# Kernel optimization log

Measured on AMD Instinct MI355X. Metric: run time of the kernel, lower is better.

The kernel has to match this reference:

```python
import jax, jax.numpy as jnp
import numpy as np
import math

B = 2048
INPUT_SIZE = 1024
OUTPUT_SIZE = 512
SPONGE = 1024
ACT = 256
REC = 256
STORE = ACT + REC  # 512
DEPTH = 8
BDEPTH = 10
NEUTRAL_C = 1.0
SQRT2 = math.sqrt(2.0)


def _make_structure():
    # Deterministic stand-in for the module's random.sample-based recall wiring.
    rng = np.random.RandomState(0)
    half = (SPONGE + 1) // 2
    shuffle_perm = np.array([i // 2 + (i % 2) * half for i in range(SPONGE)], dtype=np.int64)
    unused = []
    recall = []
    for i in range(DEPTH):
        unused.extend(range(i * STORE, (i + 1) * STORE))
        sel = rng.choice(len(unused), size=REC, replace=False)
        sel_set = set(sel.tolist())
        recall.append([unused[k] for k in sorted(sel_set)])
        unused = [u for k, u in enumerate(unused) if k not in sel_set]
    out_mem = np.array(sorted(unused), dtype=np.int64)  # 2048 leftover memory columns
    bf_size = len(out_mem) + SPONGE  # 3072
    bf_depth = int(math.ceil(math.log2(bf_size)))  # 12
    bf_half = (bf_size + 1) // 2
    bf_perm = np.array([i // 2 + (i % 2) * bf_half for i in range(bf_size)], dtype=np.int64)
    return shuffle_perm, np.array(recall, dtype=np.int64), out_mem, bf_perm, bf_size, bf_depth


def setup_inputs() -> dict:
    key = jax.random.key(0)
    ks = jax.random.split(key, 6)
    shuffle_perm, recall_idx, out_mem_idx, bf_perm, bf_size, bf_depth = _make_structure()
    return {
        "X": jax.random.normal(ks[0], (B, INPUT_SIZE), jnp.float32),
        "scales": jnp.ones((INPUT_SIZE,), jnp.float32),
        "angles": jax.random.uniform(ks[1], (DEPTH, BDEPTH, SPONGE // 2), jnp.float32) * (2 * math.pi),
        "act_bias": jax.random.normal(ks[2], (DEPTH, ACT), jnp.float32),
        "act_activation": jax.random.normal(ks[3], (DEPTH, ACT), jnp.float32),
        "act_curvature": jax.random.normal(ks[4], (DEPTH, ACT), jnp.float32),
        "bf_angles": jax.random.uniform(ks[5], (bf_depth, bf_size // 2), jnp.float32) * (2 * math.pi),
        "shuffle_perm": jnp.asarray(shuffle_perm),
        "recall_idx": jnp.asarray(recall_idx),
        "output_mem_idx": jnp.asarray(out_mem_idx),
        "bf_perm": jnp.asarray(bf_perm),
    }


def _base_activation(x, c):
    # In the source, `a` is overwritten with torch.tensor(1.0), so a == 1.
    t = (math.pi / 4) / c
    y0 = (1.0 / c) * (1.0 / SQRT2 - math.cos(math.pi / 2))  # = 1/(c*sqrt(2))
    m0 = math.sin(math.pi / 2)  # = 1
    y1 = (1.0 / c) * (1.0 / SQRT2 - 1.0)
    m1 = math.sin(0.0)  # = 0
    mid = (1.0 / c) * (1.0 / SQRT2 - jnp.cos(math.pi / 4 + c * x))
    return jnp.where(x > t, y0 + m0 * (x - t), jnp.where(x < -t, y1 + m1 * (x + t), mid))


def _butterfly(x, angles, perm):
    # angles: [n_layers, exch]; shuffle -> Givens rotation per pair, extra passthrough
    exch = angles.shape[1]
    for j in range(angles.shape[0]):
        s = x[:, perm]
        x1, x2 = s[:, :exch], s[:, exch:2 * exch]
        ca, sa = jnp.cos(angles[j]), jnp.sin(angles[j])
        x = jnp.concatenate([ca * x1 + sa * x2, -sa * x1 + ca * x2, s[:, 2 * exch:]], axis=1)
    return x


def reference(X, scales, angles, act_bias, act_activation, act_curvature, bf_angles,
              shuffle_perm, recall_idx, output_mem_idx, bf_perm):
    Xs = X * scales
    sponge = Xs[:, :SPONGE]  # input_size == sponge_size: no zero pad, memory[0] is empty
    mem = jnp.zeros((Xs.shape[0], DEPTH * STORE), Xs.dtype)
    for i in range(DEPTH):
        sponge = _butterfly(sponge, angles[i], shuffle_perm)
        x1 = sponge[:, STORE:STORE + ACT] + act_bias[i]  # activation_position == store_size
        c = 0.5 * NEUTRAL_C * (act_curvature[i] + jnp.sqrt(act_curvature[i] ** 2 + 1.0))
        ap = _base_activation(x1, c)
        am = _base_activation(-x1, c)
        act_out = jnp.stack([ap, am], axis=2).reshape(ap.shape[0], 2 * ACT)  # interleave +/-
        mem = mem.at[:, i * STORE:(i + 1) * STORE].set(sponge[:, :STORE])
        recall = mem[:, recall_idx[i]]  # indices only address already-filled columns
        # [act_out | sponge[store:act_pos] (empty) | sponge[act_pos+ACT:] | recall]
        sponge = jnp.concatenate([act_out, sponge[:, STORE + ACT:], recall], axis=1)
    pre = jnp.concatenate([mem[:, output_mem_idx], sponge], axis=1)  # [B, 3072]
    out = _butterfly(pre, bf_angles, bf_perm)
    return out[:, :OUTPUT_SIZE]
```

## Files before the change

### kernel.cpp

```cpp
#include <hip/hip_runtime.h>
#include <math.h>

#define NB 2048
#define DEPTH 8

#define FTAB_OFF    0
#define BF01_OFF    81920
#define BFF_OFF     88064
#define ACT4_OFF    98304
#define PHYSA_OFF   106496
#define PHYSR_OFF   110592
#define PHYSO2_OFF  112640

#define MB0 4608
#define MB1 6656

#define SBAR() asm volatile("s_waitcnt lgkmcnt(0)\n\ts_barrier" ::: "memory")

__global__ void setup_kernel(const float* __restrict__ angles,
                             const float* __restrict__ bf_angles,
                             const float* __restrict__ act_bias,
                             const float* __restrict__ act_curv,
                             const int* __restrict__ recall_idx,
                             const int* __restrict__ out_mem_idx,
                             float* __restrict__ ws) {
    __shared__ int physL[4096];
    __shared__ int rcl[2048];
    __shared__ int oml[2048];
    if (blockIdx.x < 200) {
        int id = blockIdx.x * 256 + threadIdx.x;
        if (id < 40960) {
            int w = id & 3, t = (id >> 2) & 255, dg = id >> 10;
            int d = dg / 5, g = dg - 5 * d;
            int a = 2 * (t & 127) + (t >> 7);
            int pair = (w == 0) ? a : (w == 1) ? (a + 256)
                     : (w == 2) ? (2 * a) : (2 * a + 1);
            int st = 2 * g + (w >> 1);
            float ang = angles[(d * 10 + st) * 512 + pair];
            float s, c; __sincosf(ang, &s, &c);
            ws[FTAB_OFF + 2 * id]     = c;
            ws[FTAB_OFF + 2 * id + 1] = s;
        } else if (id < 44032) {
            int e = id - 40960;
            int w = e & 3; int ti = e >> 2;
            int t = ti / 3; int i = ti - 3 * t;
            int a = t + 256 * i;
            int pair = (w == 0) ? a : (w == 1) ? (a + 768)
                     : (w == 2) ? (2 * a) : (2 * a + 1);
            int stage = (w < 2) ? 0 : 1;
            float ang = bf_angles[stage * 1536 + pair];
            float s, c; __sincosf(ang, &s, &c);
            ws[BF01_OFF + 2 * e]     = c;
            ws[BF01_OFF + 2 * e + 1] = s;
        } else if (id < 49152) {
            int e = id - 44032;
            int f = e >> 10; int rem = e & 1023; int t = rem >> 2; int w = rem & 3;
            int P;
            if (f == 0) P = 3 * t;
            else if (f < 4) { int k = 8 - 2 * f;
                              P = ((t >> (2 * f)) * (768 >> k)) + (t & ((256 >> k) - 1)); }
            else P = t;
            int pair = (w == 0) ? P : (w == 1) ? (P + 768)
                     : (w == 2) ? (2 * P) : (2 * P + 1);
            int stage = (w < 2) ? (2 + 2 * f) : (3 + 2 * f);
            float ang = bf_angles[stage * 1536 + pair];
            float s, c; __sincosf(ang, &s, &c);
            ws[BFF_OFF + 2 * e]     = c;
            ws[BFF_OFF + 2 * e + 1] = s;
        } else if (id < 51200) {
            int ida = id - 49152;
            float cu = act_curv[ida];
            float c  = 0.5f * (cu + sqrtf(cu * cu + 1.0f));
            ((float4*)(ws + ACT4_OFF))[ida] =
                make_float4(act_bias[ida], c, 1.0f / c, 0.0f);
        }
    } else {
        int tid = threadIdx.x;
        for (int e = tid; e < 2048; e += 256) rcl[e] = recall_idx[e];
        for (int e = tid; e < 2048; e += 256) oml[e] = out_mem_idx[e];
        for (int e = tid; e < 512; e += 256) physL[e] = e;
        __syncthreads();
        for (int d = 1; d < 8; ++d) {
            for (int j = tid; j < 512; j += 256) {
                int p;
                if (j < 256) p = 256 + d * 256 + j;
                else          p = physL[rcl[(d - 1) * 256 + (j - 256)]];
                physL[512 * d + j] = p;
            }
            __syncthreads();
        }
        int* pa = (int*)(ws + PHYSA_OFF);
        for (int e = tid; e < 2048; e += 256) {
            int d = e >> 8, t = e & 255;
            int a = 2 * (t & 127) + (t >> 7);
            pa[2 * e]     = 2 * physL[d * 512 + 2 * a];
            pa[2 * e + 1] = 2 * physL[d * 512 + 2 * a + 1];
        }
        int* pr = (int*)(ws + PHYSR_OFF);
        for (int e = tid; e < 2048; e += 256)
            pr[e] = 2 * physL[rcl[e]];
        int* po = (int*)(ws + PHYSO2_OFF);
        for (int e = tid; e < 3072; e += 256) {
            int tt = e / 12; int r = e - 12 * tt; int i = r >> 2; int k = r & 3;
            int a = tt + 256 * i;
            int tl2 = a >> 1, th2 = a & 1;
            int pos = tl2 + 1536 * th2 + 384 * k;
            po[e] = (pos < 2048) ? 2 * physL[oml[pos]]
                                 : MB0 + 2 * (pos - 2048);
        }
    }
}

__device__ __forceinline__ float actf(float x, float c, float ic) {
    const float is2 = 0.70710678118654752f;
    float tt = 0.78539816339744831f * ic;
    float y0 = is2 * ic;
    float y1 = (is2 - 1.0f) * ic;
    float mid = ic * (is2 - __cosf(0.78539816339744831f + c * x));
    return x > tt ? (y0 + (x - tt)) : (x < -tt ? y1 : mid);
}

__launch_bounds__(256, 4)
__global__ void sponge_kernel(const float* __restrict__ X,
                              const float* __restrict__ scales,
                              const float* __restrict__ ws,
                              float* __restrict__ out) {
    __shared__ float L[8704];
    const int t = threadIdx.x;
    const int rowA = blockIdx.x * 2;

    const float4* bf01  = (const float4*)(ws + BF01_OFF);
    const float4* bff   = (const float4*)(ws + BFF_OFF);
    const float4* act4  = (const float4*)(ws + ACT4_OFF);
    const int2* physA  = (const int2*)(ws + PHYSA_OFF);
    const int*  physr  = (const int*)(ws + PHYSR_OFF);
    const int*  physo2 = (const int*)(ws + PHYSO2_OFF);

    const int tl = t & 127, th = t >> 7;
    const int b  = tl + th * 512;
    const int a  = 2 * tl + th;
    const int Wb = 2 * (tl & 15) + 32 * th + 64 * (tl >> 4);
    const int Rb = (tl & 1) + 2 * ((tl >> 2) & 15) + 32 * ((tl >> 1) & 1)
                 + 64 * (tl >> 6) + 512 * th;
    const int WI = 2 * Wb;
    const int RI = 2 * Rb;
    const int u  = t - 128;

    float hA0, hA1, hA2, hA3, hB0, hB1, hB2, hB3;
    {
        const float* Xr0 = X + (size_t)rowA * 1024;
        const float* Xr1 = Xr0 + 1024;
        float s0 = scales[b],       s1 = scales[b + 128];
        float s2 = scales[b + 256], s3 = scales[b + 384];
        hA0 = Xr0[b] * s0; hA1 = Xr0[b + 128] * s1;
        hA2 = Xr0[b + 256] * s2; hA3 = Xr0[b + 384] * s3;
        hB0 = Xr1[b] * s0; hB1 = Xr1[b + 128] * s1;
        hB2 = Xr1[b + 256] * s2; hB3 = Xr1[b + 384] * s3;
    }

    int woff = MB0, roff = MB1;
    const float4* ft = (const float4*)(ws + FTAB_OFF) + 2 * t;
    float4 csA = ft[0], csB = ft[1];

#define DQUAD(cA, cB, i0, i1, i2, i3, F0, F1, F2, F3)                    \
    { float g0 =  (cA).x * (i0) + (cA).y * (i2);                         \
      float g2 = -(cA).y * (i0) + (cA).x * (i2);                         \
      float g1 =  (cA).z * (i1) + (cA).w * (i3);                         \
      float g3 = -(cA).w * (i1) + (cA).z * (i3);                         \
      F0 =  (cB).x * g0 + (cB).y * g1;                                   \
      F2 = -(cB).y * g0 + (cB).x * g1;                                   \
      F1 =  (cB).z * g2 + (cB).w * g3;                                   \
      F3 = -(cB).w * g2 + (cB).z * g3; }

    for (int d = 0; d < DEPTH; ++d) {
        for (int g = 0; g < 5; ++g) {
            float fA0, fA1, fA2, fA3, fB0, fB1, fB2, fB3;
            DQUAD(csA, csB, hA0, hA1, hA2, hA3, fA0, fA1, fA2, fA3);
            DQUAD(csA, csB, hB0, hB1, hB2, hB3, fB0, fB1, fB2, fB3);
            if (g < 4) {
                *(float4*)(L + woff + WI)        = make_float4(fA0, fB0, fA1, fB1);
                *(float4*)(L + woff + WI + 1024) = make_float4(fA2, fB2, fA3, fB3);
                { int tmp = woff; woff = roff; roff = tmp; }
                ft += 512;
                float4 nA = ft[0], nB = ft[1];
                SBAR();
                float2 e0 = *(const float2*)(L + roff + RI);
                float2 e1 = *(const float2*)(L + roff + RI + 256);
                float2 e2 = *(const float2*)(L + roff + RI + 512);
                float2 e3 = *(const float2*)(L + roff + RI + 768);
                hA0 = e0.x; hB0 = e0.y; hA1 = e1.x; hB1 = e1.y;
                hA2 = e2.x; hB2 = e2.y; hA3 = e3.x; hB3 = e3.y;
                csA = nA; csB = nB;
            } else {
                int2 pm = physA[d * 256 + t];
                *(float2*)(L + pm.x) = make_float2(fA0, fB0);
                *(float2*)(L + pm.y) = make_float2(fA1, fB1);
                *(float4*)(L + woff + 4 * a) = make_float4(fA2, fB2, fA3, fB3);
                { int tmp = woff; woff = roff; roff = tmp; }
                ft += 512;
                float4 nA = ft[0], nB = ft[1];
                int r0 = 0, r1 = 0;
                float4 a0, a1, a2, a3;
                if (t < 128) {
                    int k0 = t >> 1;
                    a0 = act4[d * 256 + k0];
                    a1 = act4[d * 256 + k0 + 64];
                    a2 = act4[d * 256 + k0 + 128];
                    a3 = act4[d * 256 + k0 + 192];
                } else {
                    r0 = physr[d * 256 + u];
                    r1 = physr[d * 256 + u + 128];
                }
                SBAR();
                const float* Z = L + roff;
                if (t < 128) {
                    int k0 = t >> 1;
                    float sgn = (t & 1) ? -1.0f : 1.0f;
                    float2 z0 = *(const float2*)(Z + 2 * k0);
                    float2 z1 = *(const float2*)(Z + 2 * k0 + 128);
                    float2 z2 = *(const float2*)(Z + 2 * k0 + 256);
                    float2 z3 = *(const float2*)(Z + 2 * k0 + 384);
                    hA0 = actf(sgn * (z0.x + a0.x), a0.y, a0.z);
                    hB0 = actf(sgn * (z0.y + a0.x), a0.y, a0.z);
                    hA1 = actf(sgn * (z1.x + a1.x), a1.y, a1.z);
                    hB1 = actf(sgn * (z1.y + a1.x), a1.y, a1.z);
                    hA2 = actf(sgn * (z2.x + a2.x), a2.y, a2.z);
                    hB2 = actf(sgn * (z2.y + a2.x), a2.y, a2.z);
                    hA3 = actf(sgn * (z3.x + a3.x), a3.y, a3.z);
                    hB3 = actf(sgn * (z3.y + a3.x), a3.y, a3.z);
                } else {
                    float2 k0v = *(const float2*)(Z + 512 + 2 * u);
                    float2 k1v = *(const float2*)(Z + 768 + 2 * u);
                    float2 rc0 = *(const float2*)(L + r0);
                    float2 rc1 = *(const float2*)(L + r1);
                    hA0 = k0v.x; hB0 = k0v.y;
                    hA1 = k1v.x; hB1 = k1v.y;
                    hA2 = rc0.x; hB2 = rc0.y;
                    hA3 = rc1.x; hB3 = rc1.y;
                }
                csA = nA; csB = nB;
            }
        }
    }

    int4 pg0, pg1, pg2;
    {
        const int4* pgp = (const int4*)(physo2 + t * 12);
        pg0 = pgp[0]; pg1 = pgp[1]; pg2 = pgp[2];
    }
    *(float2*)(L + MB0 + 2 * b)       = make_float2(hA0, hB0);
    *(float2*)(L + MB0 + 2 * b + 256) = make_float2(hA1, hB1);
    *(float2*)(L + MB0 + 2 * b + 512) = make_float2(hA2, hB2);
    *(float2*)(L + MB0 + 2 * b + 768) = make_float2(hA3, hB3);
    SBAR();

    float2 w0, w1, w2, w3, w4, w5, w6, w7, w8, w9, w10, w11;
    w0 = *(const float2*)(L + pg0.x); w1 = *(const float2*)(L + pg0.y);
    w2 = *(const float2*)(L + pg0.z); w3 = *(const float2*)(L + pg0.w);
    w4 = *(const float2*)(L + pg1.x); w5 = *(const float2*)(L + pg1.y);
    w6 = *(const float2*)(L + pg1.z); w7 = *(const float2*)(L + pg1.w);
    w8 = *(const float2*)(L + pg2.x); w9 = *(const float2*)(L + pg2.y);
    w10 = *(const float2*)(L + pg2.z); w11 = *(const float2*)(L + pg2.w);
    SBAR();

#define BF01_STEP(i, q0, q1, q2, q3)                                                \
    {                                                                               \
        float4 c01 = bf01[(t * 3 + (i)) * 2];                                       \
        float4 c23 = bf01[(t * 3 + (i)) * 2 + 1];                                   \
        float yA0, yA1, yA2, yA3, yB0, yB1, yB2, yB3;                               \
        DQUAD(c01, c23, q0.x, q1.x, q2.x, q3.x, yA0, yA1, yA2, yA3);                \
        DQUAD(c01, c23, q0.y, q1.y, q2.y, q3.y, yB0, yB1, yB2, yB3);                \
        *(float4*)(L + 4 * t + 1024 * (i))        = make_float4(yA0, yB0, yA1, yB1);\
        *(float4*)(L + 4 * t + 1024 * (i) + 3072) = make_float4(yA2, yB2, yA3, yB3);\
    }
    BF01_STEP(0, w0, w1, w2, w3)
    BF01_STEP(1, w4, w5, w6, w7)
    BF01_STEP(2, w8, w9, w10, w11)
#undef BF01_STEP
    SBAR();

#pragma unroll
    for (int f = 0; f < 4; ++f) {
        int P;
        if (f == 0) P = 3 * t;
        else { const int k = 8 - 2 * f;
               P = ((t >> (2 * f)) * (768 >> k)) + (t & ((256 >> k) - 1)); }
        int base = 2 * ((P >> 1) + (P & 1) * 1536);
        float4 csS = bff[(f * 256 + t) * 2];
        float4 csT = bff[(f * 256 + t) * 2 + 1];
        float2 x1p = *(const float2*)(L + base);
        float2 x1q = *(const float2*)(L + base + 768);
        float2 x2p = *(const float2*)(L + base + 1536);
        float2 x2q = *(const float2*)(L + base + 2304);
        float o1P =  csS.x * x1p.x + csS.y * x2p.x;
        float o2P = -csS.y * x1p.x + csS.x * x2p.x;
        float o1Q =  csS.z * x1q.x + csS.w * x2q.x;
        float o2Q = -csS.w * x1q.x + csS.z * x2q.x;
        float yA0 =  csT.x * o1P + csT.y * o1Q;
        float yA2 = -csT.y * o1P + csT.x * o1Q;
        float yA1 =  csT.z * o2P + csT.w * o2Q;
        float yA3 = -csT.w * o2P + csT.z * o2Q;
        o1P =  csS.x * x1p.y + csS.y * x2p.y;
        o2P = -csS.y * x1p.y + csS.x * x2p.y;
        o1Q =  csS.z * x1q.y + csS.w * x2q.y;
        o2Q = -csS.w * x1q.y + csS.z * x2q.y;
        float yB0 =  csT.x * o1P + csT.y * o1Q;
        float yB2 = -csT.y * o1P + csT.x * o1Q;
        float yB1 =  csT.z * o2P + csT.w * o2Q;
        float yB3 = -csT.w * o2P + csT.z * o2Q;
        SBAR();
        *(float4*)(L + 4 * P)        = make_float4(yA0, yB0, yA1, yB1);
        *(float4*)(L + 4 * P + 3072) = make_float4(yA2, yB2, yA3, yB3);
        SBAR();
    }

    {
        int base = 2 * ((t >> 1) + (t & 1) * 1536);
        float4 csS = bff[(4 * 256 + t) * 2];
        float4 csT = bff[(4 * 256 + t) * 2 + 1];
        float2 x1p = *(const float2*)(L + base);
        float2 x1q = *(const float2*)(L + base + 768);
        float2 x2p = *(const float2*)(L + base + 1536);
        float2 x2q = *(const float2*)(L + base + 2304);
        float o1P =  csS.x * x1p.x + csS.y * x2p.x;
        float o2P = -csS.y * x1p.x + csS.x * x2p.x;
        float o1Q =  csS.z * x1q.x + csS.w * x2q.x;
        float o2Q = -csS.w * x1q.x + csS.z * x2q.x;
        *(float2*)(out + (size_t)rowA * 512 + 2 * t) =
            make_float2(csT.x * o1P + csT.y * o1Q, csT.z * o2P + csT.w * o2Q);
        o1P =  csS.x * x1p.y + csS.y * x2p.y;
        o2P = -csS.y * x1p.y + csS.x * x2p.y;
        o1Q =  csS.z * x1q.y + csS.w * x2q.y;
        o2Q = -csS.w * x1q.y + csS.z * x2q.y;
        *(float2*)(out + (size_t)(rowA + 1) * 512 + 2 * t) =
            make_float2(csT.x * o1P + csT.y * o1Q, csT.z * o2P + csT.w * o2Q);
    }
#undef DQUAD
}

extern "C" void kernel_launch(void* const* d_in, const int* in_sizes, int n_in,
                              void* d_out, int out_size, void* d_ws, size_t ws_size,
                              hipStream_t stream) {
    const float* X          = (const float*)d_in[0];
    const float* scales     = (const float*)d_in[1];
    const float* angles     = (const float*)d_in[2];
    const float* act_bias   = (const float*)d_in[3];
    const float* act_curv   = (const float*)d_in[5];
    const float* bf_angles  = (const float*)d_in[6];
    const int*   recall_idx  = (const int*)d_in[8];
    const int*   out_mem_idx = (const int*)d_in[9];

    float* ws = (float*)d_ws;

    setup_kernel<<<201, 256, 0, stream>>>(angles, bf_angles, act_bias, act_curv,
                                          recall_idx, out_mem_idx, ws);
    sponge_kernel<<<NB / 2, 256, 0, stream>>>(X, scales, ws, (float*)d_out);
}
```

Measured before the change: 113.4 us.

## Process four rows per block to amortize butterfly coefficient loads and barriers

```diff
diff --git a/kernel.cpp b/kernel.cpp
--- a/kernel.cpp
+++ b/kernel.cpp
@@ -14,6 +14,7 @@
 
 #define MB0 4608
 #define MB1 6656
+#define RD  8704
 
 #define SBAR() asm volatile("s_waitcnt lgkmcnt(0)\n\ts_barrier" ::: "memory")
 
@@ -120,14 +121,14 @@
     return x > tt ? (y0 + (x - tt)) : (x < -tt ? y1 : mid);
 }
 
-__launch_bounds__(256, 4)
+__launch_bounds__(256, 2)
 __global__ void sponge_kernel(const float* __restrict__ X,
                               const float* __restrict__ scales,
                               const float* __restrict__ ws,
                               float* __restrict__ out) {
-    __shared__ float L[8704];
+    __shared__ float L[17408];
     const int t = threadIdx.x;
-    const int rowA = blockIdx.x * 2;
+    const int rowA = blockIdx.x * 4;
 
     const float4* bf01  = (const float4*)(ws + BF01_OFF);
     const float4* bff   = (const float4*)(ws + BFF_OFF);
@@ -147,15 +148,22 @@
     const int u  = t - 128;
 
     float hA0, hA1, hA2, hA3, hB0, hB1, hB2, hB3;
+    float hC0, hC1, hC2, hC3, hD0, hD1, hD2, hD3;
     {
         const float* Xr0 = X + (size_t)rowA * 1024;
         const float* Xr1 = Xr0 + 1024;
+        const float* Xr2 = Xr0 + 2048;
+        const float* Xr3 = Xr0 + 3072;
         float s0 = scales[b],       s1 = scales[b + 128];
         float s2 = scales[b + 256], s3 = scales[b + 384];
         hA0 = Xr0[b] * s0; hA1 = Xr0[b + 128] * s1;
         hA2 = Xr0[b + 256] * s2; hA3 = Xr0[b + 384] * s3;
         hB0 = Xr1[b] * s0; hB1 = Xr1[b + 128] * s1;
         hB2 = Xr1[b + 256] * s2; hB3 = Xr1[b + 384] * s3;
+        hC0 = Xr2[b] * s0; hC1 = Xr2[b + 128] * s1;
+        hC2 = Xr2[b + 256] * s2; hC3 = Xr2[b + 384] * s3;
+        hD0 = Xr3[b] * s0; hD1 = Xr3[b + 128] * s1;
+        hD2 = Xr3[b + 256] * s2; hD3 = Xr3[b + 384] * s3;
     }
 
     int woff = MB0, roff = MB1;
@@ -175,11 +183,16 @@
     for (int d = 0; d < DEPTH; ++d) {
         for (int g = 0; g < 5; ++g) {
             float fA0, fA1, fA2, fA3, fB0, fB1, fB2, fB3;
+            float fC0, fC1, fC2, fC3, fD0, fD1, fD2, fD3;
             DQUAD(csA, csB, hA0, hA1, hA2, hA3, fA0, fA1, fA2, fA3);
             DQUAD(csA, csB, hB0, hB1, hB2, hB3, fB0, fB1, fB2, fB3);
+            DQUAD(csA, csB, hC0, hC1, hC2, hC3, fC0, fC1, fC2, fC3);
+            DQUAD(csA, csB, hD0, hD1, hD2, hD3, fD0, fD1, fD2, fD3);
             if (g < 4) {
-                *(float4*)(L + woff + WI)        = make_float4(fA0, fB0, fA1, fB1);
-                *(float4*)(L + woff + WI + 1024) = make_float4(fA2, fB2, fA3, fB3);
+                *(float4*)(L + woff + WI)             = make_float4(fA0, fB0, fA1, fB1);
+                *(float4*)(L + woff + WI + 1024)      = make_float4(fA2, fB2, fA3, fB3);
+                *(float4*)(L + woff + RD + WI)        = make_float4(fC0, fD0, fC1, fD1);
+                *(float4*)(L + woff + RD + WI + 1024) = make_float4(fC2, fD2, fC3, fD3);
                 { int tmp = woff; woff = roff; roff = tmp; }
                 ft += 512;
                 float4 nA = ft[0], nB = ft[1];
@@ -188,14 +201,23 @@
                 float2 e1 = *(const float2*)(L + roff + RI + 256);
                 float2 e2 = *(const float2*)(L + roff + RI + 512);
                 float2 e3 = *(const float2*)(L + roff + RI + 768);
+                float2 f0 = *(const float2*)(L + roff + RD + RI);
+                float2 f1 = *(const float2*)(L + roff + RD + RI + 256);
+                float2 f2 = *(const float2*)(L + roff + RD + RI + 512);
+                float2 f3 = *(const float2*)(L + roff + RD + RI + 768);
                 hA0 = e0.x; hB0 = e0.y; hA1 = e1.x; hB1 = e1.y;
                 hA2 = e2.x; hB2 = e2.y; hA3 = e3.x; hB3 = e3.y;
+                hC0 = f0.x; hD0 = f0.y; hC1 = f1.x; hD1 = f1.y;
+                hC2 = f2.x; hD2 = f2.y; hC3 = f3.x; hD3 = f3.y;
                 csA = nA; csB = nB;
             } else {
                 int2 pm = physA[d * 256 + t];
-                *(float2*)(L + pm.x) = make_float2(fA0, fB0);
-                *(float2*)(L + pm.y) = make_float2(fA1, fB1);
-                *(float4*)(L + woff + 4 * a) = make_float4(fA2, fB2, fA3, fB3);
+                *(float2*)(L + pm.x)      = make_float2(fA0, fB0);
+                *(float2*)(L + pm.y)      = make_float2(fA1, fB1);
+                *(float2*)(L + pm.x + RD) = make_float2(fC0, fD0);
+                *(float2*)(L + pm.y + RD) = make_float2(fC1, fD1);
+                *(float4*)(L + woff + 4 * a)      = make_float4(fA2, fB2, fA3, fB3);
+                *(float4*)(L + woff + RD + 4 * a) = make_float4(fC2, fD2, fC3, fD3);
                 { int tmp = woff; woff = roff; roff = tmp; }
                 ft += 512;
                 float4 nA = ft[0], nB = ft[1];
@@ -220,6 +242,10 @@
                     float2 z1 = *(const float2*)(Z + 2 * k0 + 128);
                     float2 z2 = *(const float2*)(Z + 2 * k0 + 256);
                     float2 z3 = *(const float2*)(Z + 2 * k0 + 384);
+                    float2 y0 = *(const float2*)(Z + RD + 2 * k0);
+                    float2 y1 = *(const float2*)(Z + RD + 2 * k0 + 128);
+                    float2 y2 = *(const float2*)(Z + RD + 2 * k0 + 256);
+                    float2 y3 = *(const float2*)(Z + RD + 2 * k0 + 384);
                     hA0 = actf(sgn * (z0.x + a0.x), a0.y, a0.z);
                     hB0 = actf(sgn * (z0.y + a0.x), a0.y, a0.z);
                     hA1 = actf(sgn * (z1.x + a1.x), a1.y, a1.z);
@@ -228,15 +254,31 @@
                     hB2 = actf(sgn * (z2.y + a2.x), a2.y, a2.z);
                     hA3 = actf(sgn * (z3.x + a3.x), a3.y, a3.z);
                     hB3 = actf(sgn * (z3.y + a3.x), a3.y, a3.z);
+                    hC0 = actf(sgn * (y0.x + a0.x), a0.y, a0.z);
+                    hD0 = actf(sgn * (y0.y + a0.x), a0.y, a0.z);
+                    hC1 = actf(sgn * (y1.x + a1.x), a1.y, a1.z);
+                    hD1 = actf(sgn * (y1.y + a1.x), a1.y, a1.z);
+                    hC2 = actf(sgn * (y2.x + a2.x), a2.y, a2.z);
+                    hD2 = actf(sgn * (y2.y + a2.x), a2.y, a2.z);
+                    hC3 = actf(sgn * (y3.x + a3.x), a3.y, a3.z);
+                    hD3 = actf(sgn * (y3.y + a3.x), a3.y, a3.z);
                 } else {
                     float2 k0v = *(const float2*)(Z + 512 + 2 * u);
                     float2 k1v = *(const float2*)(Z + 768 + 2 * u);
                     float2 rc0 = *(const float2*)(L + r0);
                     float2 rc1 = *(const float2*)(L + r1);
+                    float2 k2v = *(const float2*)(Z + RD + 512 + 2 * u);
+                    float2 k3v = *(const float2*)(Z + RD + 768 + 2 * u);
+                    float2 rc2 = *(const float2*)(L + r0 + RD);
+                    float2 rc3 = *(const float2*)(L + r1 + RD);
                     hA0 = k0v.x; hB0 = k0v.y;
                     hA1 = k1v.x; hB1 = k1v.y;
                     hA2 = rc0.x; hB2 = rc0.y;
                     hA3 = rc1.x; hB3 = rc1.y;
+                    hC0 = k2v.x; hD0 = k2v.y;
+                    hC1 = k3v.x; hD1 = k3v.y;
+                    hC2 = rc2.x; hD2 = rc2.y;
+                    hC3 = rc3.x; hD3 = rc3.y;
                 }
                 csA = nA; csB = nB;
             }
@@ -248,34 +290,48 @@
         const int4* pgp = (const int4*)(physo2 + t * 12);
         pg0 = pgp[0]; pg1 = pgp[1]; pg2 = pgp[2];
     }
-    *(float2*)(L + MB0 + 2 * b)       = make_float2(hA0, hB0);
-    *(float2*)(L + MB0 + 2 * b + 256) = make_float2(hA1, hB1);
-    *(float2*)(L + MB0 + 2 * b + 512) = make_float2(hA2, hB2);
-    *(float2*)(L + MB0 + 2 * b + 768) = make_float2(hA3, hB3);
+    *(float2*)(L + MB0 + 2 * b)            = make_float2(hA0, hB0);
+    *(float2*)(L + MB0 + 2 * b + 256)      = make_float2(hA1, hB1);
+    *(float2*)(L + MB0 + 2 * b + 512)      = make_float2(hA2, hB2);
+    *(float2*)(L + MB0 + 2 * b + 768)      = make_float2(hA3, hB3);
+    *(float2*)(L + MB0 + RD + 2 * b)       = make_float2(hC0, hD0);
+    *(float2*)(L + MB0 + RD + 2 * b + 256) = make_float2(hC1, hD1);
+    *(float2*)(L + MB0 + RD + 2 * b + 512) = make_float2(hC2, hD2);
+    *(float2*)(L + MB0 + RD + 2 * b + 768) = make_float2(hC3, hD3);
     SBAR();
 
     float2 w0, w1, w2, w3, w4, w5, w6, w7, w8, w9, w10, w11;
+    float2 v0, v1, v2, v3, v4, v5, v6, v7, v8, v9, v10, v11;
     w0 = *(const float2*)(L + pg0.x); w1 = *(const float2*)(L + pg0.y);
     w2 = *(const float2*)(L + pg0.z); w3 = *(const float2*)(L + pg0.w);
     w4 = *(const float2*)(L + pg1.x); w5 = *(const float2*)(L + pg1.y);
     w6 = *(const float2*)(L + pg1.z); w7 = *(const float2*)(L + pg1.w);
     w8 = *(const float2*)(L + pg2.x); w9 = *(const float2*)(L + pg2.y);
     w10 = *(const float2*)(L + pg2.z); w11 = *(const float2*)(L + pg2.w);
+    v0 = *(const float2*)(L + pg0.x + RD); v1 = *(const float2*)(L + pg0.y + RD);
+    v2 = *(const float2*)(L + pg0.z + RD); v3 = *(const float2*)(L + pg0.w + RD);
+    v4 = *(const float2*)(L + pg1.x + RD); v5 = *(const float2*)(L + pg1.y + RD);
+    v6 = *(const float2*)(L + pg1.z + RD); v7 = *(const float2*)(L + pg1.w + RD);
+    v8 = *(const float2*)(L + pg2.x + RD); v9 = *(const float2*)(L + pg2.y + RD);
+    v10 = *(const float2*)(L + pg2.z + RD); v11 = *(const float2*)(L + pg2.w + RD);
     SBAR();
 
-#define BF01_STEP(i, q0, q1, q2, q3)                                                \
+#define BF01_STEP(i, q0, q1, q2, q3, DST)                                           \
     {                                                                               \
         float4 c01 = bf01[(t * 3 + (i)) * 2];                                       \
         float4 c23 = bf01[(t * 3 + (i)) * 2 + 1];                                   \
         float yA0, yA1, yA2, yA3, yB0, yB1, yB2, yB3;                               \
         DQUAD(c01, c23, q0.x, q1.x, q2.x, q3.x, yA0, yA1, yA2, yA3);                \
         DQUAD(c01, c23, q0.y, q1.y, q2.y, q3.y, yB0, yB1, yB2, yB3);                \
-        *(float4*)(L + 4 * t + 1024 * (i))        = make_float4(yA0, yB0, yA1, yB1);\
-        *(float4*)(L + 4 * t + 1024 * (i) + 3072) = make_float4(yA2, yB2, yA3, yB3);\
-    }
-    BF01_STEP(0, w0, w1, w2, w3)
-    BF01_STEP(1, w4, w5, w6, w7)
-    BF01_STEP(2, w8, w9, w10, w11)
+        *(float4*)(L + (DST) + 4 * t + 1024 * (i))        = make_float4(yA0, yB0, yA1, yB1);\
+        *(float4*)(L + (DST) + 4 * t + 1024 * (i) + 3072) = make_float4(yA2, yB2, yA3, yB3);\
+    }
+    BF01_STEP(0, w0, w1, w2, w3, 0)
+    BF01_STEP(1, w4, w5, w6, w7, 0)
+    BF01_STEP(2, w8, w9, w10, w11, 0)
+    BF01_STEP(0, v0, v1, v2, v3, RD)
+    BF01_STEP(1, v4, v5, v6, v7, RD)
+    BF01_STEP(2, v8, v9, v10, v11, RD)
 #undef BF01_STEP
     SBAR();
 
@@ -292,6 +348,10 @@
         float2 x1q = *(const float2*)(L + base + 768);
         float2 x2p = *(const float2*)(L + base + 1536);
         float2 x2q = *(const float2*)(L + base + 2304);
+        float2 u1p = *(const float2*)(L + base + RD);
+        float2 u1q = *(const float2*)(L + base + RD + 768);
+        float2 u2p = *(const float2*)(L + base + RD + 1536);
+        float2 u2q = *(const float2*)(L + base + RD + 2304);
         float o1P =  csS.x * x1p.x + csS.y * x2p.x;
         float o2P = -csS.y * x1p.x + csS.x * x2p.x;
         float o1Q =  csS.z * x1q.x + csS.w * x2q.x;
@@ -308,9 +368,27 @@
         float yB2 = -csT.y * o1P + csT.x * o1Q;
         float yB1 =  csT.z * o2P + csT.w * o2Q;
         float yB3 = -csT.w * o2P + csT.z * o2Q;
+        o1P =  csS.x * u1p.x + csS.y * u2p.x;
+        o2P = -csS.y * u1p.x + csS.x * u2p.x;
+        o1Q =  csS.z * u1q.x + csS.w * u2q.x;
+        o2Q = -csS.w * u1q.x + csS.z * u2q.x;
+        float yC0 =  csT.x * o1P + csT.y * o1Q;
+        float yC2 = -csT.y * o1P + csT.x * o1Q;
+        float yC1 =  csT.z * o2P + csT.w * o2Q;
+        float yC3 = -csT.w * o2P + csT.z * o2Q;
+        o1P =  csS.x * u1p.y + csS.y * u2p.y;
+        o2P = -csS.y * u1p.y + csS.x * u2p.y;
+        o1Q =  csS.z * u1q.y + csS.w * u2q.y;
+        o2Q = -csS.w * u1q.y + csS.z * u2q.y;
+        float yD0 =  csT.x * o1P + csT.y * o1Q;
+        float yD2 = -csT.y * o1P + csT.x * o1Q;
+        float yD1 =  csT.z * o2P + csT.w * o2Q;
+        float yD3 = -csT.w * o2P + csT.z * o2Q;
         SBAR();
-        *(float4*)(L + 4 * P)        = make_float4(yA0, yB0, yA1, yB1);
-        *(float4*)(L + 4 * P + 3072) = make_float4(yA2, yB2, yA3, yB3);
+        *(float4*)(L + 4 * P)             = make_float4(yA0, yB0, yA1, yB1);
+        *(float4*)(L + 4 * P + 3072)      = make_float4(yA2, yB2, yA3, yB3);
+        *(float4*)(L + RD + 4 * P)        = make_float4(yC0, yD0, yC1, yD1);
+        *(float4*)(L + RD + 4 * P + 3072) = make_float4(yC2, yD2, yC3, yD3);
         SBAR();
     }
 
@@ -322,6 +400,10 @@
         float2 x1q = *(const float2*)(L + base + 768);
         float2 x2p = *(const float2*)(L + base + 1536);
         float2 x2q = *(const float2*)(L + base + 2304);
+        float2 u1p = *(const float2*)(L + base + RD);
+        float2 u1q = *(const float2*)(L + base + RD + 768);
+        float2 u2p = *(const float2*)(L + base + RD + 1536);
+        float2 u2q = *(const float2*)(L + base + RD + 2304);
         float o1P =  csS.x * x1p.x + csS.y * x2p.x;
         float o2P = -csS.y * x1p.x + csS.x * x2p.x;
         float o1Q =  csS.z * x1q.x + csS.w * x2q.x;
@@ -334,6 +416,18 @@
         o2Q = -csS.w * x1q.y + csS.z * x2q.y;
         *(float2*)(out + (size_t)(rowA + 1) * 512 + 2 * t) =
             make_float2(csT.x * o1P + csT.y * o1Q, csT.z * o2P + csT.w * o2Q);
+        o1P =  csS.x * u1p.x + csS.y * u2p.x;
+        o2P = -csS.y * u1p.x + csS.x * u2p.x;
+        o1Q =  csS.z * u1q.x + csS.w * u2q.x;
+        o2Q = -csS.w * u1q.x + csS.z * u2q.x;
+        *(float2*)(out + (size_t)(rowA + 2) * 512 + 2 * t) =
+            make_float2(csT.x * o1P + csT.y * o1Q, csT.z * o2P + csT.w * o2Q);
+        o1P =  csS.x * u1p.y + csS.y * u2p.y;
+        o2P = -csS.y * u1p.y + csS.x * u2p.y;
+        o1Q =  csS.z * u1q.y + csS.w * u2q.y;
+        o2Q = -csS.w * u1q.y + csS.z * u2q.y;
+        *(float2*)(out + (size_t)(rowA + 3) * 512 + 2 * t) =
+            make_float2(csT.x * o1P + csT.y * o1Q, csT.z * o2P + csT.w * o2Q);
     }
 #undef DQUAD
 }
@@ -354,5 +448,5 @@
 
     setup_kernel<<<201, 256, 0, stream>>>(angles, bf_angles, act_bias, act_curv,
                                           recall_idx, out_mem_idx, ws);
-    sponge_kernel<<<NB / 2, 256, 0, stream>>>(X, scales, ws, (float*)d_out);
+    sponge_kernel<<<NB / 4, 256, 0, stream>>>(X, scales, ws, (float*)d_out);
 }
```

Result: slower. 119.6 us (+5.5%).

## Process one batch row per block instead of two, halving shared memory

Applied to the files above, without the earlier changes.

```diff
diff --git a/kernel.cpp b/kernel.cpp
--- a/kernel.cpp
+++ b/kernel.cpp
@@ -12,8 +12,8 @@
 #define PHYSR_OFF   110592
 #define PHYSO2_OFF  112640
 
-#define MB0 4608
-#define MB1 6656
+#define MB0 2304
+#define MB1 3328
 
 #define SBAR() asm volatile("s_waitcnt lgkmcnt(0)\n\ts_barrier" ::: "memory")
 
@@ -93,20 +93,20 @@
         for (int e = tid; e < 2048; e += 256) {
             int d = e >> 8, t = e & 255;
             int a = 2 * (t & 127) + (t >> 7);
-            pa[2 * e]     = 2 * physL[d * 512 + 2 * a];
-            pa[2 * e + 1] = 2 * physL[d * 512 + 2 * a + 1];
+            pa[2 * e]     = physL[d * 512 + 2 * a];
+            pa[2 * e + 1] = physL[d * 512 + 2 * a + 1];
         }
         int* pr = (int*)(ws + PHYSR_OFF);
         for (int e = tid; e < 2048; e += 256)
-            pr[e] = 2 * physL[rcl[e]];
+            pr[e] = physL[rcl[e]];
         int* po = (int*)(ws + PHYSO2_OFF);
         for (int e = tid; e < 3072; e += 256) {
             int tt = e / 12; int r = e - 12 * tt; int i = r >> 2; int k = r & 3;
             int a = tt + 256 * i;
             int tl2 = a >> 1, th2 = a & 1;
             int pos = tl2 + 1536 * th2 + 384 * k;
-            po[e] = (pos < 2048) ? 2 * physL[oml[pos]]
-                                 : MB0 + 2 * (pos - 2048);
+            po[e] = (pos < 2048) ? physL[oml[pos]]
+                                 : MB0 + (pos - 2048);
         }
     }
 }
@@ -120,14 +120,14 @@
     return x > tt ? (y0 + (x - tt)) : (x < -tt ? y1 : mid);
 }
 
-__launch_bounds__(256, 4)
+__launch_bounds__(256, 8)
 __global__ void sponge_kernel(const float* __restrict__ X,
                               const float* __restrict__ scales,
                               const float* __restrict__ ws,
                               float* __restrict__ out) {
-    __shared__ float L[8704];
+    __shared__ float L[4352];
     const int t = threadIdx.x;
-    const int rowA = blockIdx.x * 2;
+    const int row = blockIdx.x;
 
     const float4* bf01  = (const float4*)(ws + BF01_OFF);
     const float4* bff   = (const float4*)(ws + BFF_OFF);
@@ -139,23 +139,18 @@
     const int tl = t & 127, th = t >> 7;
     const int b  = tl + th * 512;
     const int a  = 2 * tl + th;
-    const int Wb = 2 * (tl & 15) + 32 * th + 64 * (tl >> 4);
-    const int Rb = (tl & 1) + 2 * ((tl >> 2) & 15) + 32 * ((tl >> 1) & 1)
+    const int Wn = 2 * (tl & 15) + 32 * th + 64 * (tl >> 4);
+    const int Rn = (tl & 1) + 2 * ((tl >> 2) & 15) + 32 * ((tl >> 1) & 1)
                  + 64 * (tl >> 6) + 512 * th;
-    const int WI = 2 * Wb;
-    const int RI = 2 * Rb;
     const int u  = t - 128;
 
-    float hA0, hA1, hA2, hA3, hB0, hB1, hB2, hB3;
+    float h0, h1, h2, h3;
     {
-        const float* Xr0 = X + (size_t)rowA * 1024;
-        const float* Xr1 = Xr0 + 1024;
-        float s0 = scales[b],       s1 = scales[b + 128];
-        float s2 = scales[b + 256], s3 = scales[b + 384];
-        hA0 = Xr0[b] * s0; hA1 = Xr0[b + 128] * s1;
-        hA2 = Xr0[b + 256] * s2; hA3 = Xr0[b + 384] * s3;
-        hB0 = Xr1[b] * s0; hB1 = Xr1[b + 128] * s1;
-        hB2 = Xr1[b + 256] * s2; hB3 = Xr1[b + 384] * s3;
+        const float* Xr = X + (size_t)row * 1024;
+        h0 = Xr[b]       * scales[b];
+        h1 = Xr[b + 128] * scales[b + 128];
+        h2 = Xr[b + 256] * scales[b + 256];
+        h3 = Xr[b + 384] * scales[b + 384];
     }
 
     int woff = MB0, roff = MB1;
@@ -174,28 +169,25 @@
 
     for (int d = 0; d < DEPTH; ++d) {
         for (int g = 0; g < 5; ++g) {
-            float fA0, fA1, fA2, fA3, fB0, fB1, fB2, fB3;
-            DQUAD(csA, csB, hA0, hA1, hA2, hA3, fA0, fA1, fA2, fA3);
-            DQUAD(csA, csB, hB0, hB1, hB2, hB3, fB0, fB1, fB2, fB3);
+            float f0, f1, f2, f3;
+            DQUAD(csA, csB, h0, h1, h2, h3, f0, f1, f2, f3);
             if (g < 4) {
-                *(float4*)(L + woff + WI)        = make_float4(fA0, fB0, fA1, fB1);
-                *(float4*)(L + woff + WI + 1024) = make_float4(fA2, fB2, fA3, fB3);
+                *(float2*)(L + woff + Wn)       = make_float2(f0, f1);
+                *(float2*)(L + woff + Wn + 512) = make_float2(f2, f3);
                 { int tmp = woff; woff = roff; roff = tmp; }
                 ft += 512;
                 float4 nA = ft[0], nB = ft[1];
                 SBAR();
-                float2 e0 = *(const float2*)(L + roff + RI);
-                float2 e1 = *(const float2*)(L + roff + RI + 256);
-                float2 e2 = *(const float2*)(L + roff + RI + 512);
-                float2 e3 = *(const float2*)(L + roff + RI + 768);
-                hA0 = e0.x; hB0 = e0.y; hA1 = e1.x; hB1 = e1.y;
-                hA2 = e2.x; hB2 = e2.y; hA3 = e3.x; hB3 = e3.y;
+                h0 = L[roff + Rn];
+                h1 = L[roff + Rn + 128];
+                h2 = L[roff + Rn + 256];
+                h3 = L[roff + Rn + 384];
                 csA = nA; csB = nB;
             } else {
                 int2 pm = physA[d * 256 + t];
-                *(float2*)(L + pm.x) = make_float2(fA0, fB0);
-                *(float2*)(L + pm.y) = make_float2(fA1, fB1);
-                *(float4*)(L + woff + 4 * a) = make_float4(fA2, fB2, fA3, fB3);
+                L[pm.x] = f0;
+                L[pm.y] = f1;
+                *(float2*)(L + woff + 2 * a) = make_float2(f2, f3);
                 { int tmp = woff; woff = roff; roff = tmp; }
                 ft += 512;
                 float4 nA = ft[0], nB = ft[1];
@@ -216,27 +208,19 @@
                 if (t < 128) {
                     int k0 = t >> 1;
                     float sgn = (t & 1) ? -1.0f : 1.0f;
-                    float2 z0 = *(const float2*)(Z + 2 * k0);
-                    float2 z1 = *(const float2*)(Z + 2 * k0 + 128);
-                    float2 z2 = *(const float2*)(Z + 2 * k0 + 256);
-                    float2 z3 = *(const float2*)(Z + 2 * k0 + 384);
-                    hA0 = actf(sgn * (z0.x + a0.x), a0.y, a0.z);
-                    hB0 = actf(sgn * (z0.y + a0.x), a0.y, a0.z);
-                    hA1 = actf(sgn * (z1.x + a1.x), a1.y, a1.z);
-                    hB1 = actf(sgn * (z1.y + a1.x), a1.y, a1.z);
-                    hA2 = actf(sgn * (z2.x + a2.x), a2.y, a2.z);
-                    hB2 = actf(sgn * (z2.y + a2.x), a2.y, a2.z);
-                    hA3 = actf(sgn * (z3.x + a3.x), a3.y, a3.z);
-                    hB3 = actf(sgn * (z3.y + a3.x), a3.y, a3.z);
+                    float z0 = Z[k0];
+                    float z1 = Z[k0 + 64];
+                    float z2 = Z[k0 + 128];
+                    float z3 = Z[k0 + 192];
+                    h0 = actf(sgn * (z0 + a0.x), a0.y, a0.z);
+                    h1 = actf(sgn * (z1 + a1.x), a1.y, a1.z);
+                    h2 = actf(sgn * (z2 + a2.x), a2.y, a2.z);
+                    h3 = actf(sgn * (z3 + a3.x), a3.y, a3.z);
                 } else {
-                    float2 k0v = *(const float2*)(Z + 512 + 2 * u);
-                    float2 k1v = *(const float2*)(Z + 768 + 2 * u);
-                    float2 rc0 = *(const float2*)(L + r0);
-                    float2 rc1 = *(const float2*)(L + r1);
-                    hA0 = k0v.x; hB0 = k0v.y;
-                    hA1 = k1v.x; hB1 = k1v.y;
-                    hA2 = rc0.x; hB2 = rc0.y;
-                    hA3 = rc1.x; hB3 = rc1.y;
+                    h0 = Z[256 + u];
+                    h1 = Z[384 + u];
+                    h2 = L[r0];
+                    h3 = L[r1];
                 }
                 csA = nA; csB = nB;
             }
@@ -248,30 +232,26 @@
         const int4* pgp = (const int4*)(physo2 + t * 12);
         pg0 = pgp[0]; pg1 = pgp[1]; pg2 = pgp[2];
     }
-    *(float2*)(L + MB0 + 2 * b)       = make_float2(hA0, hB0);
-    *(float2*)(L + MB0 + 2 * b + 256) = make_float2(hA1, hB1);
-    *(float2*)(L + MB0 + 2 * b + 512) = make_float2(hA2, hB2);
-    *(float2*)(L + MB0 + 2 * b + 768) = make_float2(hA3, hB3);
+    L[MB0 + b]       = h0;
+    L[MB0 + b + 128] = h1;
+    L[MB0 + b + 256] = h2;
+    L[MB0 + b + 384] = h3;
     SBAR();
 
-    float2 w0, w1, w2, w3, w4, w5, w6, w7, w8, w9, w10, w11;
-    w0 = *(const float2*)(L + pg0.x); w1 = *(const float2*)(L + pg0.y);
-    w2 = *(const float2*)(L + pg0.z); w3 = *(const float2*)(L + pg0.w);
-    w4 = *(const float2*)(L + pg1.x); w5 = *(const float2*)(L + pg1.y);
-    w6 = *(const float2*)(L + pg1.z); w7 = *(const float2*)(L + pg1.w);
-    w8 = *(const float2*)(L + pg2.x); w9 = *(const float2*)(L + pg2.y);
-    w10 = *(const float2*)(L + pg2.z); w11 = *(const float2*)(L + pg2.w);
+    float w0, w1, w2, w3, w4, w5, w6, w7, w8, w9, w10, w11;
+    w0 = L[pg0.x]; w1 = L[pg0.y]; w2 = L[pg0.z]; w3 = L[pg0.w];
+    w4 = L[pg1.x]; w5 = L[pg1.y]; w6 = L[pg1.z]; w7 = L[pg1.w];
+    w8 = L[pg2.x]; w9 = L[pg2.y]; w10 = L[pg2.z]; w11 = L[pg2.w];
     SBAR();
 
-#define BF01_STEP(i, q0, q1, q2, q3)                                                \
-    {                                                                               \
-        float4 c01 = bf01[(t * 3 + (i)) * 2];                                       \
-        float4 c23 = bf01[(t * 3 + (i)) * 2 + 1];                                   \
-        float yA0, yA1, yA2, yA3, yB0, yB1, yB2, yB3;                               \
-        DQUAD(c01, c23, q0.x, q1.x, q2.x, q3.x, yA0, yA1, yA2, yA3);                \
-        DQUAD(c01, c23, q0.y, q1.y, q2.y, q3.y, yB0, yB1, yB2, yB3);                \
-        *(float4*)(L + 4 * t + 1024 * (i))        = make_float4(yA0, yB0, yA1, yB1);\
-        *(float4*)(L + 4 * t + 1024 * (i) + 3072) = make_float4(yA2, yB2, yA3, yB3);\
+#define BF01_STEP(i, q0, q1, q2, q3)                                     \
+    {                                                                    \
+        float4 c01 = bf01[(t * 3 + (i)) * 2];                            \
+        float4 c23 = bf01[(t * 3 + (i)) * 2 + 1];                        \
+        float y0, y1, y2, y3;                                            \
+        DQUAD(c01, c23, q0, q1, q2, q3, y0, y1, y2, y3);                 \
+        *(float2*)(L + 2 * t + 512 * (i))        = make_float2(y0, y1);  \
+        *(float2*)(L + 2 * t + 512 * (i) + 1536) = make_float2(y2, y3);  \
     }
     BF01_STEP(0, w0, w1, w2, w3)
     BF01_STEP(1, w4, w5, w6, w7)
@@ -285,54 +265,40 @@
         if (f == 0) P = 3 * t;
         else { const int k = 8 - 2 * f;
                P = ((t >> (2 * f)) * (768 >> k)) + (t & ((256 >> k) - 1)); }
-        int base = 2 * ((P >> 1) + (P & 1) * 1536);
+        int base = (P >> 1) + (P & 1) * 1536;
         float4 csS = bff[(f * 256 + t) * 2];
         float4 csT = bff[(f * 256 + t) * 2 + 1];
-        float2 x1p = *(const float2*)(L + base);
-        float2 x1q = *(const float2*)(L + base + 768);
-        float2 x2p = *(const float2*)(L + base + 1536);
-        float2 x2q = *(const float2*)(L + base + 2304);
-        float o1P =  csS.x * x1p.x + csS.y * x2p.x;
-        float o2P = -csS.y * x1p.x + csS.x * x2p.x;
-        float o1Q =  csS.z * x1q.x + csS.w * x2q.x;
-        float o2Q = -csS.w * x1q.x + csS.z * x2q.x;
-        float yA0 =  csT.x * o1P + csT.y * o1Q;
-        float yA2 = -csT.y * o1P + csT.x * o1Q;
-        float yA1 =  csT.z * o2P + csT.w * o2Q;
-        float yA3 = -csT.w * o2P + csT.z * o2Q;
-        o1P =  csS.x * x1p.y + csS.y * x2p.y;
-        o2P = -csS.y * x1p.y + csS.x * x2p.y;
-        o1Q =  csS.z * x1q.y + csS.w * x2q.y;
-        o2Q = -csS.w * x1q.y + csS.z * x2q.y;
-        float yB0 =  csT.x * o1P + csT.y * o1Q;
-        float yB2 = -csT.y * o1P + csT.x * o1Q;
-        float yB1 =  csT.z * o2P + csT.w * o2Q;
-        float yB3 = -csT.w * o2P + csT.z * o2Q;
+        float x1p = L[base];
+        float x1q = L[base + 384];
+        float x2p = L[base + 768];
+        float x2q = L[base + 1152];
+        float o1P =  csS.x * x1p + csS.y * x2p;
+        float o2P = -csS.y * x1p + csS.x * x2p;
+        float o1Q =  csS.z * x1q + csS.w * x2q;
+        float o2Q = -csS.w * x1q + csS.z * x2q;
+        float y0 =  csT.x * o1P + csT.y * o1Q;
+        float y2 = -csT.y * o1P + csT.x * o1Q;
+        float y1 =  csT.z * o2P + csT.w * o2Q;
+        float y3 = -csT.w * o2P + csT.z * o2Q;
         SBAR();
-        *(float4*)(L + 4 * P)        = make_float4(yA0, yB0, yA1, yB1);
-        *(float4*)(L + 4 * P + 3072) = make_float4(yA2, yB2, yA3, yB3);
+        *(float2*)(L + 2 * P)        = make_float2(y0, y1);
+        *(float2*)(L + 2 * P + 1536) = make_float2(y2, y3);
         SBAR();
     }
 
     {
-        int base = 2 * ((t >> 1) + (t & 1) * 1536);
+        int base = (t >> 1) + (t & 1) * 1536;
         float4 csS = bff[(4 * 256 + t) * 2];
         float4 csT = bff[(4 * 256 + t) * 2 + 1];
-        float2 x1p = *(const float2*)(L + base);
-        float2 x1q = *(const float2*)(L + base + 768);
-        float2 x2p = *(const float2*)(L + base + 1536);
-        float2 x2q = *(const float2*)(L + base + 2304);
-        float o1P =  csS.x * x1p.x + csS.y * x2p.x;
-        float o2P = -csS.y * x1p.x + csS.x * x2p.x;
-        float o1Q =  csS.z * x1q.x + csS.w * x2q.x;
-        float o2Q = -csS.w * x1q.x + csS.z * x2q.x;
-        *(float2*)(out + (size_t)rowA * 512 + 2 * t) =
-            make_float2(csT.x * o1P + csT.y * o1Q, csT.z * o2P + csT.w * o2Q);
-        o1P =  csS.x * x1p.y + csS.y * x2p.y;
-        o2P = -csS.y * x1p.y + csS.x * x2p.y;
-        o1Q =  csS.z * x1q.y + csS.w * x2q.y;
-        o2Q = -csS.w * x1q.y + csS.z * x2q.y;
-        *(float2*)(out + (size_t)(rowA + 1) * 512 + 2 * t) =
+        float x1p = L[base];
+        float x1q = L[base + 384];
+        float x2p = L[base + 768];
+        float x2q = L[base + 1152];
+        float o1P =  csS.x * x1p + csS.y * x2p;
+        float o2P = -csS.y * x1p + csS.x * x2p;
+        float o1Q =  csS.z * x1q + csS.w * x2q;
+        float o2Q = -csS.w * x1q + csS.z * x2q;
+        *(float2*)(out + (size_t)row * 512 + 2 * t) =
             make_float2(csT.x * o1P + csT.y * o1Q, csT.z * o2P + csT.w * o2Q);
     }
 #undef DQUAD
@@ -354,5 +320,5 @@
 
     setup_kernel<<<201, 256, 0, stream>>>(angles, bf_angles, act_bias, act_curv,
                                           recall_idx, out_mem_idx, ws);
-    sponge_kernel<<<NB / 2, 256, 0, stream>>>(X, scales, ws, (float*)d_out);
+    sponge_kernel<<<NB, 256, 0, stream>>>(X, scales, ws, (float*)d_out);
 }
```

Measured after the change: 123.5 us. 8.9% more time.
